# Kernel tuning notes

Measured on AMD Instinct MI355X. Metric: run time of the kernel, lower is better.

Reference implementation:

```python
import jax, jax.numpy as jnp
import numpy as np

B, N_PER_G, F, E_PER_G = 16, 2048, 1024, 65536
NUM_STEPS = 64
BARRIER = 0.1
INIT_TAU = 1.0
TAU_SCALE = 0.5
STEP_ALPHA = 1.0


def setup_inputs() -> dict:
    key = jax.random.key(0)
    ks = jax.random.split(key, 8)
    N = B * N_PER_G
    E = B * E_PER_G
    x_start = jax.random.uniform(ks[0], (N,), dtype=jnp.float32) + 0.1  # strictly interior (x > 0)
    rhs = jax.random.uniform(ks[1], (N,), dtype=jnp.float32)
    proj_matrix = jax.random.normal(ks[2], (B, N_PER_G, F), dtype=jnp.float32) / np.sqrt(N_PER_G)
    q = jax.random.normal(ks[3], (N,), dtype=jnp.float32)
    obj_solution = jax.random.uniform(ks[4], (B,), dtype=jnp.float32) + 0.5  # nonzero denominators
    # per-graph edges: local indices in [0, n) then offset by graph id * n
    local = jax.random.randint(ks[5], (2, B, E_PER_G), 0, N_PER_G)
    offsets = (jnp.arange(B) * N_PER_G)[None, :, None]
    edge_index = (local + offsets).reshape(2, E).astype(jnp.int64)
    edge_weight = jax.random.normal(ks[6], (E,), dtype=jnp.float32)
    vals_batch = jnp.repeat(jnp.arange(B), N_PER_G).astype(jnp.int64)
    return {"x_start": x_start, "rhs": rhs, "proj_matrix": proj_matrix, "q": q,
            "obj_solution": obj_solution, "edge_index": edge_index,
            "edge_weight": edge_weight, "vals_batch": vals_batch}


def reference(x_start, rhs, proj_matrix, q, obj_solution, edge_index, edge_weight, vals_batch):
    src, dst = edge_index[0], edge_index[1]
    ebatch = vals_batch[src]  # graph id per edge

    def qp_obj(x):
        quad = jax.ops.segment_sum(edge_weight * x[src] * x[dst], ebatch, num_segments=B)
        lin = (q * x).reshape(B, N_PER_G).sum(axis=1)
        return 0.5 * quad + lin

    def step(carry, _):
        x, best_x, best_obj, tau = carry
        direction = (-x + rhs) + BARRIER * tau / (x + tau)
        tau = jnp.maximum(tau * TAU_SCALE, 1e-5)
        # null-space projection: pred = P (P^T d), P orthonormal basis [B, n, f]
        d = direction.reshape(B, N_PER_G)
        coef = jnp.einsum('bnf,bn->bf', proj_matrix, d)
        pred = jnp.einsum('bnf,bf->bn', proj_matrix, coef).reshape(-1)
        # batched line search: largest alpha <= step_alpha keeping x + alpha*pred >= 0
        neg = pred < 0
        denom = jnp.where(neg, -pred, 1.0)  # safe division
        ratio = jnp.where(neg, x / denom, STEP_ALPHA)
        alpha_g = jnp.minimum(ratio.reshape(B, N_PER_G).min(axis=1), STEP_ALPHA)
        alpha = alpha_g[vals_batch] * 0.995
        x = x + alpha * pred
        cur = qp_obj(x)
        better = cur < best_obj
        best_obj = jnp.where(better, cur, best_obj)
        best_x = jnp.where(better[vals_batch], x, best_x)
        return (x, best_x, best_obj, tau), best_obj

    best_obj0 = qp_obj(x_start)
    init = (x_start, x_start, best_obj0, jnp.float32(INIT_TAU))
    (x_fin, best_x, best_obj, _), objs = jax.lax.scan(step, init, None, length=NUM_STEPS)
    obj_gaps = objs.T  # [B, T]
    opt = obj_solution[:, None]
    obj_gaps = jnp.abs((opt - obj_gaps) / opt)
    best = jnp.abs((obj_solution - best_obj) / obj_solution)
    return (best_x, best, obj_gaps)
```

## Files before the change

### kernel.cpp

```cpp
#include <hip/hip_runtime.h>

#define BATCHES 16
#define NG 2048
#define FDIM 1024
#define EPG 65536
#define NTOT (BATCHES*NG)
#define ETOT (BATCHES*EPG)
#define STEPS 64
#define NBLK 512
#define NTHR 512
#define WAVES (NTHR/64)
#define BLK_PER_BATCH (NBLK/BATCHES)
#define ROWS_PER_BLK (NG/BLK_PER_BATCH)
#define EDGE_PER_BLK (ETOT/NBLK)
#define EDGES_PER_THR (EDGE_PER_BLK/NTHR)

#define WS_XB0   0
#define WS_XB1   (NTOT)
#define WS_PRED  (2*NTOT)
#define WS_COEF  (3*NTOT)
#define WS_QUAD  (3*NTOT + 2*BATCHES*FDIM)
#define WS_LIN   (WS_QUAD + 2*BATCHES)
#define WS_MINR  (WS_LIN + 2*BATCHES)
#define WS_BAR   (WS_MINR + 2*BATCHES)

__device__ unsigned long long g_bbar[BATCHES][8];

__device__ __forceinline__ double ld_ag(const double* p) {
    return __hip_atomic_load(p, __ATOMIC_RELAXED, __HIP_MEMORY_SCOPE_AGENT);
}
__device__ __forceinline__ void st_ag(double* p, double v) {
    __hip_atomic_store(p, v, __ATOMIC_RELAXED, __HIP_MEMORY_SCOPE_AGENT);
}
__device__ __forceinline__ unsigned long long ldu64_ag(const unsigned long long* p) {
    return __hip_atomic_load(p, __ATOMIC_RELAXED, __HIP_MEMORY_SCOPE_AGENT);
}
__device__ __forceinline__ void stu64_ag(unsigned long long* p, unsigned long long v) {
    __hip_atomic_store(p, v, __ATOMIC_RELAXED, __HIP_MEMORY_SCOPE_AGENT);
}

__device__ __forceinline__ void batch_barrier(unsigned long long* bb,
                                              unsigned long long g, int tid) {
    asm volatile("s_waitcnt vmcnt(0)" ::: "memory");
    __syncthreads();
    if (tid == 0) {
        unsigned long long old = __hip_atomic_fetch_add(
            &bb[0], 1ULL, __ATOMIC_RELAXED, __HIP_MEMORY_SCOPE_AGENT);
        if (old == (unsigned long long)BLK_PER_BATCH * g - 1ULL) {
            stu64_ag(&bb[1], g);
        } else {
            while (ldu64_ag(&bb[1]) < g) __builtin_amdgcn_s_sleep(2);
        }
    }
    __syncthreads();
}

__device__ __forceinline__ double block_reduce_sum(double v, double* s_red) {
    for (int off = 32; off > 0; off >>= 1)
        v += __shfl_down(v, off, 64);
    __syncthreads();
    int lane = threadIdx.x & 63;
    int wave = threadIdx.x >> 6;
    if (lane == 0) s_red[wave] = v;
    __syncthreads();
    double s = 0.0;
    #pragma unroll
    for (int w = 0; w < WAVES; ++w) s += s_red[w];
    return s;
}

__global__ __launch_bounds__(NTHR, 4)
void GradSolver_58102317580919_kernel(
    const float* __restrict__ x_start,
    const float* __restrict__ rhs,
    const float* __restrict__ proj,
    const float* __restrict__ q,
    const float* __restrict__ obj_solution,
    const int*   __restrict__ edge_index,
    const float* __restrict__ edge_weight,
    float* __restrict__ out,
    void* __restrict__ wsv)
{
    double* ws = (double*)wsv;
    double* xb[2] = { ws + WS_XB0, ws + WS_XB1 };
    double* pred  = ws + WS_PRED;
    double* coef  = ws + WS_COEF;
    double* quad  = ws + WS_QUAD;
    double* lin   = ws + WS_LIN;
    unsigned long long* minr = (unsigned long long*)(ws + WS_MINR);

    const int tid   = threadIdx.x;
    const int bid   = blockIdx.x;
    const int batch = bid / BLK_PER_BATCH;
    const int lbid  = bid % BLK_PER_BATCH;
    const int row_base = batch * NG + lbid * ROWS_PER_BLK;
    const int nbase = batch * NG;
    const int lane  = tid & 63;
    const int wave  = tid >> 6;

    unsigned long long* bb = &g_bbar[batch][0];

    const unsigned long long DINF = 0x7FF0000000000000ULL;

    __shared__ double s_d[ROWS_PER_BLK];
    __shared__ double s_x[ROWS_PER_BLK];
    __shared__ double s_pred[ROWS_PER_BLK];
    __shared__ double s_coef[FDIM];
    __shared__ double s_xp[NG];
    __shared__ double s_red[WAVES];
    __shared__ double s_bestobj;

    unsigned long long g = 0;
    double tau = 1.0;

    unsigned epk[EDGES_PER_THR];
    float    ew[EDGES_PER_THR];
    {
        const int e0 = bid * EDGE_PER_BLK;
        #pragma unroll
        for (int j = 0; j < EDGES_PER_THR; ++j) {
            int e = e0 + tid + j*NTHR;
            unsigned si = (unsigned)(edge_index[e]        - nbase);
            unsigned di = (unsigned)(edge_index[ETOT + e] - nbase);
            epk[j] = si | (di << 11);
            ew[j]  = edge_weight[e];
        }
    }

    if (tid < 32) {
        st_ag(&coef[0*(BATCHES*FDIM) + batch*FDIM + lbid*32 + tid], 0.0);
        st_ag(&coef[1*(BATCHES*FDIM) + batch*FDIM + lbid*32 + tid], 0.0);
    }
    if (lbid == 0 && tid == 0) {
        st_ag(&quad[batch], 0.0);      st_ag(&quad[16+batch], 0.0);
        st_ag(&lin[batch],  0.0);      st_ag(&lin[16+batch],  0.0);
        stu64_ag(&minr[batch], DINF);  stu64_ag(&minr[16+batch], DINF);
    }
    if (tid == 0) s_bestobj = __longlong_as_double((long long)DINF);
    batch_barrier(bb, ++g, tid);

    for (int k = 0; k <= STEPS; ++k) {
        const int p  = k & 1;
        const int pp = 1 - p;
        double alpha = 0.0;
        if (k > 0) {
            unsigned long long m = ldu64_ag(&minr[pp*16 + batch]);
            alpha = fmin(__longlong_as_double((long long)m), 1.0) * 0.995;
        }
        double sxr[NG/NTHR], spr[NG/NTHR];
        if (k > 0) {
            const double* xprev = xb[pp];
            #pragma unroll
            for (int j = 0; j < NG/NTHR; ++j) {
                sxr[j] = ld_ag(&xprev[nbase + tid + j*NTHR]);
                spr[j] = ld_ag(&pred[nbase + tid + j*NTHR]);
            }
        }
        double xv = 0.0;
        if (tid < ROWS_PER_BLK) {
            xv = (k == 0) ? (double)x_start[row_base + tid]
                          : s_x[tid] + alpha * s_pred[tid];
            s_x[tid] = xv;
            st_ag(&xb[p][row_base + tid], xv);
            if (k < STEPS)
                s_d[tid] = -xv + (double)rhs[row_base + tid] + 0.1 * tau / (xv + tau);
        }
        tau = fmax(tau * 0.5, 1e-5);

        if (k == 0) {
            #pragma unroll
            for (int j = 0; j < NG/NTHR; ++j) {
                int i = tid + j*NTHR;
                s_xp[i] = (double)x_start[nbase + i];
            }
        } else {
            #pragma unroll
            for (int j = 0; j < NG/NTHR; ++j)
                s_xp[tid + j*NTHR] = sxr[j] + alpha * spr[j];
        }

        if (k >= 1 && tid < 32)
            st_ag(&coef[pp*(BATCHES*FDIM) + batch*FDIM + lbid*32 + tid], 0.0);
        if (k < STEPS && lbid == 0 && tid == 0)
            stu64_ag(&minr[p*16 + batch], DINF);

        __syncthreads();

        if (tid < 64) {
            double lp = (double)q[row_base + tid] * xv;
            for (int off = 32; off > 0; off >>= 1)
                lp += __shfl_down(lp, off, 64);
            if (tid == 0) unsafeAtomicAdd(&lin[p*16 + batch], lp);
        }

        {
            double qp = 0.0;
            #pragma unroll
            for (int j = 0; j < EDGES_PER_THR; ++j) {
                unsigned pk = epk[j];
                qp += (double)ew[j] * s_xp[pk & 2047u] * s_xp[(pk >> 11) & 2047u];
            }
            double qs = block_reduce_sum(qp, s_red);
            if (tid == 0) unsafeAtomicAdd(&quad[p*16 + batch], qs);
        }

        if (k < STEPS) {
            double a0 = 0.0, a1 = 0.0;
            const float2* P2 = (const float2*)(proj + (size_t)row_base * FDIM);
            #pragma unroll 8
            for (int r = 0; r < ROWS_PER_BLK; ++r) {
                float2 pv = P2[r*(FDIM/2) + tid];
                double dv = s_d[r];
                a0 += (double)pv.x * dv;
                a1 += (double)pv.y * dv;
            }
            double* cf = coef + p*(BATCHES*FDIM) + batch*FDIM + 2*tid;
            unsafeAtomicAdd(cf+0, a0);
            unsafeAtomicAdd(cf+1, a1);
        }
        batch_barrier(bb, ++g, tid);

        double cv0 = 0.0, cv1 = 0.0;
        if (k < STEPS) {
            cv0 = ld_ag(&coef[p*(BATCHES*FDIM) + batch*FDIM + tid]);
            cv1 = ld_ag(&coef[p*(BATCHES*FDIM) + batch*FDIM + tid + NTHR]);
        }
        double qv = ld_ag(&quad[p*16 + batch]);
        double lv = ld_ag(&lin[p*16 + batch]);

        double wmin = 1e300;
        if (k < STEPS) {
            s_coef[tid]        = cv0;
            s_coef[tid + NTHR] = cv1;
            __syncthreads();
            double c[16];
            #pragma unroll
            for (int j = 0; j < 4; ++j) {
                int f = 4*(lane + 64*j);
                c[4*j+0] = s_coef[f+0]; c[4*j+1] = s_coef[f+1];
                c[4*j+2] = s_coef[f+2]; c[4*j+3] = s_coef[f+3];
            }
            for (int i = 0; i < ROWS_PER_BLK/WAVES; ++i) {
                int r  = wave * (ROWS_PER_BLK/WAVES) + i;
                int gr = row_base + r;
                const float4* Pr = (const float4*)(proj + (size_t)gr * FDIM);
                double dot = 0.0;
                #pragma unroll
                for (int j = 0; j < 4; ++j) {
                    float4 pv = Pr[lane + 64*j];
                    dot += (double)pv.x*c[4*j+0] + (double)pv.y*c[4*j+1]
                         + (double)pv.z*c[4*j+2] + (double)pv.w*c[4*j+3];
                }
                for (int off = 32; off > 0; off >>= 1)
                    dot += __shfl_down(dot, off, 64);
                if (lane == 0) {
                    s_pred[r] = dot;
                    st_ag(&pred[gr], dot);
                    if (dot < 0.0) wmin = fmin(wmin, s_x[r] / (-dot));
                }
            }
            if (lane == 0) s_red[wave] = wmin;
        }

        double cur = 0.5 * qv + lv;
        double bo  = s_bestobj;
        bool better = cur < bo;
        double nb2 = better ? cur : bo;
        __syncthreads();
        if (tid == 0) s_bestobj = nb2;
        if (k < STEPS && tid == 0) {
            double m8 = s_red[0];
            #pragma unroll
            for (int w = 1; w < WAVES; ++w) m8 = fmin(m8, s_red[w]);
            atomicMin(&minr[p*16 + batch],
                      (unsigned long long)__double_as_longlong(m8));
        }
        if (k < STEPS && lbid == 0 && tid == 0) {
            st_ag(&quad[pp*16 + batch], 0.0);
            st_ag(&lin[pp*16 + batch],  0.0);
        }
        if (lbid == 0 && tid == 0) {
            double opt = (double)obj_solution[batch];
            double gap = fabs((opt - nb2)/opt);
            if (k >= 1)     out[NTOT + BATCHES + batch*STEPS + (k-1)] = (float)gap;
            if (k == STEPS) out[NTOT + batch] = (float)gap;
        }
        if (better && tid < ROWS_PER_BLK)
            out[row_base + tid] = (float)s_x[tid];

        if (k == STEPS) break;
        batch_barrier(bb, ++g, tid);
    }
}

extern "C" void kernel_launch(void* const* d_in, const int* in_sizes, int n_in,
                              void* d_out, int out_size, void* d_ws, size_t ws_size,
                              hipStream_t stream) {
    const float* x_start      = (const float*)d_in[0];
    const float* rhs          = (const float*)d_in[1];
    const float* proj         = (const float*)d_in[2];
    const float* q            = (const float*)d_in[3];
    const float* obj_solution = (const float*)d_in[4];
    const int*   edge_index   = (const int*)d_in[5];
    const float* edge_weight  = (const float*)d_in[6];
    float* out = (float*)d_out;
    void* ws   = d_ws;

    void* bbar_ptr = nullptr;
    hipGetSymbolAddress(&bbar_ptr, HIP_SYMBOL(g_bbar));
    hipMemsetAsync(bbar_ptr, 0, sizeof(unsigned long long) * BATCHES * 8, stream);

    hipLaunchKernelGGL(GradSolver_58102317580919_kernel,
                       dim3(NBLK), dim3(NTHR), 0, stream,
                       x_start, rhs, proj, q, obj_solution,
                       edge_index, edge_weight, out, ws);
}
```

Measured before the change: 4.525 ms.

## Keep projection rows in registers across steps and reuse column layout for back-projection

Each thread now loads 32 of its block's 64 projection rows (float2 per row) into registers once, before the step loop, and reuses them for both the forward (P^T d) and backward (P coef) products in every step. The back-projection is reorganized to use the same per-thread column pair as the forward pass: each thread multiplies its two coefficients, reduces within the wave, and the per-wave partial sums are combined through shared memory. This replaces the old row-per-wave float4 scheme and removes the shared coef staging. The goal is to cut repeated global/L2 reads of the projection matrix. The cost is much higher register pressure, which risks spills under the 4-block launch bound, plus 64 wave reductions per step.

```diff
diff --git a/kernel.cpp b/kernel.cpp
--- a/kernel.cpp
+++ b/kernel.cpp
@@ -14,6 +14,7 @@
 #define ROWS_PER_BLK (NG/BLK_PER_BATCH)
 #define EDGE_PER_BLK (ETOT/NBLK)
 #define EDGES_PER_THR (EDGE_PER_BLK/NTHR)
+#define REGROWS 32
 
 #define WS_XB0   0
 #define WS_XB1   (NTOT)
@@ -68,6 +69,17 @@
     for (int w = 0; w < WAVES; ++w) s += s_red[w];
     return s;
 }
+
+__device__ __forceinline__ void row_reduce(double cr, int r, int lane, int wave,
+                                           double* s_pp) {
+    for (int off = 32; off > 0; off >>= 1)
+        cr += __shfl_down(cr, off, 64);
+    if (lane == 0) s_pp[wave*ROWS_PER_BLK + r] = cr;
+}
+
+#define R32(M) M(0) M(1) M(2) M(3) M(4) M(5) M(6) M(7) M(8) M(9) M(10) M(11) \
+    M(12) M(13) M(14) M(15) M(16) M(17) M(18) M(19) M(20) M(21) M(22) M(23) \
+    M(24) M(25) M(26) M(27) M(28) M(29) M(30) M(31)
 
 __global__ __launch_bounds__(NTHR, 4)
 void GradSolver_58102317580919_kernel(
@@ -105,13 +117,19 @@
     __shared__ double s_d[ROWS_PER_BLK];
     __shared__ double s_x[ROWS_PER_BLK];
     __shared__ double s_pred[ROWS_PER_BLK];
-    __shared__ double s_coef[FDIM];
     __shared__ double s_xp[NG];
+    __shared__ double s_pp[WAVES*ROWS_PER_BLK];
     __shared__ double s_red[WAVES];
     __shared__ double s_bestobj;
 
     unsigned long long g = 0;
     double tau = 1.0;
+
+    const float2* P2 = (const float2*)(proj + (size_t)row_base * FDIM);
+
+    #define DECLR(i) float2 pr##i = P2[(i)*(FDIM/2) + tid];
+    R32(DECLR)
+    #undef DECLR
 
     unsigned epk[EDGES_PER_THR];
     float    ew[EDGES_PER_THR];
@@ -147,15 +165,6 @@
             unsigned long long m = ldu64_ag(&minr[pp*16 + batch]);
             alpha = fmin(__longlong_as_double((long long)m), 1.0) * 0.995;
         }
-        double sxr[NG/NTHR], spr[NG/NTHR];
-        if (k > 0) {
-            const double* xprev = xb[pp];
-            #pragma unroll
-            for (int j = 0; j < NG/NTHR; ++j) {
-                sxr[j] = ld_ag(&xprev[nbase + tid + j*NTHR]);
-                spr[j] = ld_ag(&pred[nbase + tid + j*NTHR]);
-            }
-        }
         double xv = 0.0;
         if (tid < ROWS_PER_BLK) {
             xv = (k == 0) ? (double)x_start[row_base + tid]
@@ -174,9 +183,12 @@
                 s_xp[i] = (double)x_start[nbase + i];
             }
         } else {
+            const double* xprev = xb[pp];
             #pragma unroll
-            for (int j = 0; j < NG/NTHR; ++j)
-                s_xp[tid + j*NTHR] = sxr[j] + alpha * spr[j];
+            for (int j = 0; j < NG/NTHR; ++j) {
+                int i = tid + j*NTHR;
+                s_xp[i] = ld_ag(&xprev[nbase + i]) + alpha * ld_ag(&pred[nbase + i]);
+            }
         }
 
         if (k >= 1 && tid < 32)
@@ -206,9 +218,12 @@
 
         if (k < STEPS) {
             double a0 = 0.0, a1 = 0.0;
-            const float2* P2 = (const float2*)(proj + (size_t)row_base * FDIM);
+            #define P1R(i) { double dv = s_d[i]; \
+                a0 += (double)pr##i.x * dv; a1 += (double)pr##i.y * dv; }
+            R32(P1R)
+            #undef P1R
             #pragma unroll 8
-            for (int r = 0; r < ROWS_PER_BLK; ++r) {
+            for (int r = REGROWS; r < ROWS_PER_BLK; ++r) {
                 float2 pv = P2[r*(FDIM/2) + tid];
                 double dv = s_d[r];
                 a0 += (double)pv.x * dv;
@@ -220,46 +235,25 @@
         }
         batch_barrier(bb, ++g, tid);
 
-        double cv0 = 0.0, cv1 = 0.0;
+        double c0 = 0.0, c1 = 0.0;
         if (k < STEPS) {
-            cv0 = ld_ag(&coef[p*(BATCHES*FDIM) + batch*FDIM + tid]);
-            cv1 = ld_ag(&coef[p*(BATCHES*FDIM) + batch*FDIM + tid + NTHR]);
+            c0 = ld_ag(&coef[p*(BATCHES*FDIM) + batch*FDIM + 2*tid]);
+            c1 = ld_ag(&coef[p*(BATCHES*FDIM) + batch*FDIM + 2*tid + 1]);
         }
         double qv = ld_ag(&quad[p*16 + batch]);
         double lv = ld_ag(&lin[p*16 + batch]);
 
-        double wmin = 1e300;
         if (k < STEPS) {
-            s_coef[tid]        = cv0;
-            s_coef[tid + NTHR] = cv1;
-            __syncthreads();
-            double c[16];
-            #pragma unroll
-            for (int j = 0; j < 4; ++j) {
-                int f = 4*(lane + 64*j);
-                c[4*j+0] = s_coef[f+0]; c[4*j+1] = s_coef[f+1];
-                c[4*j+2] = s_coef[f+2]; c[4*j+3] = s_coef[f+3];
-            }
-            for (int i = 0; i < ROWS_PER_BLK/WAVES; ++i) {
-                int r  = wave * (ROWS_PER_BLK/WAVES) + i;
-                int gr = row_base + r;
-                const float4* Pr = (const float4*)(proj + (size_t)gr * FDIM);
-                double dot = 0.0;
-                #pragma unroll
-                for (int j = 0; j < 4; ++j) {
-                    float4 pv = Pr[lane + 64*j];
-                    dot += (double)pv.x*c[4*j+0] + (double)pv.y*c[4*j+1]
-                         + (double)pv.z*c[4*j+2] + (double)pv.w*c[4*j+3];
-                }
-                for (int off = 32; off > 0; off >>= 1)
-                    dot += __shfl_down(dot, off, 64);
-                if (lane == 0) {
-                    s_pred[r] = dot;
-                    st_ag(&pred[gr], dot);
-                    if (dot < 0.0) wmin = fmin(wmin, s_x[r] / (-dot));
-                }
-            }
-            if (lane == 0) s_red[wave] = wmin;
+            #define P2R(i) { double cr = (double)pr##i.x * c0 + (double)pr##i.y * c1; \
+                row_reduce(cr, i, lane, wave, s_pp); }
+            R32(P2R)
+            #undef P2R
+            #pragma unroll 4
+            for (int r = REGROWS; r < ROWS_PER_BLK; ++r) {
+                float2 pv = P2[r*(FDIM/2) + tid];
+                double cr = (double)pv.x * c0 + (double)pv.y * c1;
+                row_reduce(cr, r, lane, wave, s_pp);
+            }
         }
 
         double cur = 0.5 * qv + lv;
@@ -268,12 +262,24 @@
         double nb2 = better ? cur : bo;
         __syncthreads();
         if (tid == 0) s_bestobj = nb2;
-        if (k < STEPS && tid == 0) {
-            double m8 = s_red[0];
-            #pragma unroll
-            for (int w = 1; w < WAVES; ++w) m8 = fmin(m8, s_red[w]);
-            atomicMin(&minr[p*16 + batch],
-                      (unsigned long long)__double_as_longlong(m8));
+
+        if (k < STEPS) {
+            double wmin = 1e300;
+            if (tid < ROWS_PER_BLK) {
+                double pr_ = 0.0;
+                #pragma unroll
+                for (int w = 0; w < WAVES; ++w) pr_ += s_pp[w*ROWS_PER_BLK + tid];
+                s_pred[tid] = pr_;
+                st_ag(&pred[row_base + tid], pr_);
+                if (pr_ < 0.0) wmin = fmin(wmin, s_x[tid] / (-pr_));
+            }
+            if (tid < 64) {
+                for (int off = 32; off > 0; off >>= 1)
+                    wmin = fmin(wmin, __shfl_down(wmin, off, 64));
+                if (tid == 0)
+                    atomicMin(&minr[p*16 + batch],
+                              (unsigned long long)__double_as_longlong(wmin));
+            }
         }
         if (k < STEPS && lbid == 0 && tid == 0) {
             st_ag(&quad[pp*16 + batch], 0.0);
```

Result: slower. 5.534 ms (+22.3%).
